# Performance work log

Hardware: AMD Instinct MI355X
Metric: run time of the kernel (lower is better)

Reference implementation:

```python
import jax, jax.numpy as jnp
import numpy as np

PULSE = (0.01, 0.005)
W_RGB, W_INTER, W_DIST, W_HASH = 1.0, 1.0, 0.01, 0.1
NUM_SEGMENTS = 65536
R, N = 4096, 48


def setup_inputs() -> dict:
    key = jax.random.key(0)
    ks = jax.random.split(key, 12)
    M = R * N
    return {
        "pd_rgbs": jax.random.uniform(ks[0], (R, 3), jnp.float32),
        "gt_rgbs": jax.random.uniform(ks[1], (R, 3), jnp.float32),
        "render_sdist": jnp.sort(jax.random.uniform(ks[2], (R, N + 1), jnp.float32), axis=-1),
        "render_weights": jax.random.uniform(ks[3], (R, N), jnp.float32) * 0.05,
        "prop_sdist_0": jnp.sort(jax.random.uniform(ks[4], (R, 257), jnp.float32), axis=-1),
        "prop_weights_0": jax.random.uniform(ks[5], (R, 256), jnp.float32) * 0.02,
        "prop_sdist_1": jnp.sort(jax.random.uniform(ks[6], (R, 97), jnp.float32), axis=-1),
        "prop_weights_1": jax.random.uniform(ks[7], (R, 96), jnp.float32) * 0.02,
        "enc_embds_0": jax.random.normal(ks[8], (M, 2), jnp.float32) * 0.01,
        "enc_embds_1": jax.random.normal(ks[9], (M, 2), jnp.float32) * 0.01,
        "enc_idx_0": jnp.sort(jax.random.randint(ks[10], (M,), 0, NUM_SEGMENTS)),
        "enc_idx_1": jnp.sort(jax.random.randint(ks[11], (M,), 0, NUM_SEGMENTS)),
    }


def blur_step_function(sdist, wnorm, pw):
    # sdist: [R, N+1], wnorm: [R, N]
    cat = jnp.concatenate([sdist - pw, sdist + pw], axis=-1)        # [R, 2N+2]
    sort_idx = jnp.argsort(cat, axis=-1)
    bounds = jnp.take_along_axis(cat, sort_idx, axis=-1)
    z = jnp.zeros_like(wnorm[..., :1])
    diff = jnp.concatenate([wnorm, z], -1) - jnp.concatenate([z, wnorm], -1)  # [R, N+1]
    radio = diff / (2.0 * pw)
    radio_double = jnp.concatenate([radio, -radio], axis=-1)        # [R, 2N+2]
    radio_sorted = jnp.take_along_axis(radio_double, sort_idx[..., :-1], axis=-1)
    ds = bounds[..., 1:] - bounds[..., :-1]                          # [R, 2N+1]
    recover = jnp.maximum(jnp.cumsum(ds * jnp.cumsum(radio_sorted, -1), -1), 0.0)
    blur_w = jnp.concatenate([jnp.zeros_like(recover[..., :1]), recover], -1)  # [R, 2N+2]
    return bounds, blur_w


def sorted_interp_quad(x, xp, fpdf, fcdf):
    # x: [R, X], xp/fpdf/fcdf: [R, P]
    mask = x[..., None, :] >= xp[..., :, None]  # [R, P, X]

    def find_interval(v):
        lo = jnp.where(mask, v[..., None], v[..., :1, None])
        hi = jnp.where(~mask, v[..., None], v[..., -1:, None])
        return lo.max(-2), hi.min(-2), lo.argmax(-2), hi.argmin(-2)

    fcdf0, fcdf1, i0, i1 = find_interval(fcdf)
    fpdf0 = jnp.take_along_axis(fpdf, i0, axis=-1)
    fpdf1 = jnp.take_along_axis(fpdf, i1, axis=-1)
    xp0, xp1, _, _ = find_interval(xp)
    offset = jnp.clip(jnp.nan_to_num((x - xp0) / (xp1 - xp0), nan=0.0), 0.0, 1.0)
    return fcdf0 + (x - xp0) * (fpdf0 + fpdf1 * offset + fpdf0 * (1.0 - offset)) / 2.0


def inter_loss_level(prop_sdist, prop_weights, render_sdist, wnorm, pw):
    dist_b, w_b = blur_step_function(render_sdist, wnorm, pw)
    area = 0.5 * (w_b[..., 1:] + w_b[..., :-1]) * (dist_b[..., 1:] - dist_b[..., :-1])
    cdf = jnp.concatenate([jnp.zeros_like(area[..., :1]), jnp.cumsum(area, -1)], -1)
    cdf_interp = sorted_interp_quad(prop_sdist, dist_b, w_b, cdf)
    w_s = jnp.diff(cdf_interp, axis=-1)
    return jnp.mean(jnp.maximum(w_s - prop_weights, 0.0) ** 2 / (prop_weights + 1e-5))


def distortion_loss(render_weights, render_sdist):
    mid = 0.5 * (render_sdist[..., 1:] + render_sdist[..., :-1])     # [R, N]
    sdist_all = jnp.abs(mid[..., :, None] - mid[..., None, :])       # [R, N, N]
    part1 = jnp.einsum('rn,rnm,rm->r', render_weights, sdist_all, render_weights)
    part2 = jnp.sum(render_weights ** 2 * (render_sdist[..., 1:] - render_sdist[..., :-1]), -1) / 3.0
    return jnp.mean(jnp.abs(part1) + jnp.abs(part2))


def hash_decay_level(param, idx):
    s = jax.ops.segment_sum(param ** 2, idx, num_segments=NUM_SEGMENTS)
    cnt = jax.ops.segment_sum(jnp.ones((param.shape[0], 1), param.dtype), idx, num_segments=NUM_SEGMENTS)
    return jnp.mean(s / jnp.maximum(cnt, 1.0))  # empty segments contribute 0 (like segment_coo mean init=0)


def reference(pd_rgbs, gt_rgbs, render_sdist, render_weights,
              prop_sdist_0, prop_weights_0, prop_sdist_1, prop_weights_1,
              enc_embds_0, enc_embds_1, enc_idx_0, enc_idx_1):
    loss_rgb = jnp.mean((pd_rgbs - gt_rgbs) ** 2)
    wnorm = render_weights / (render_sdist[..., 1:] - render_sdist[..., :-1] + 1e-8)
    loss_inter = (inter_loss_level(prop_sdist_0, prop_weights_0, render_sdist, wnorm, PULSE[0])
                  + inter_loss_level(prop_sdist_1, prop_weights_1, render_sdist, wnorm, PULSE[1]))
    loss_dist = distortion_loss(render_weights, render_sdist)
    loss_hash = hash_decay_level(enc_embds_0, enc_idx_0) + hash_decay_level(enc_embds_1, enc_idx_1)
    return W_RGB * loss_rgb + W_INTER * loss_inter + W_DIST * loss_dist + W_HASH * loss_hash
```

## Files before the change

kernel.cpp:

```cpp
#include <hip/hip_runtime.h>

#define R 4096
#define NN 48
#define NP 49
#define C 98
#define NSEG 65536
#define MM (R * NN)
#define RPB 4
#define GB_ROW (R / RPB)
#define GB_HASH (MM / 256)
#define GRID (GB_ROW + 2 * GB_HASH)

#define WAVE_FENCE() __builtin_amdgcn_wave_barrier()

__device__ __forceinline__ float wscan_add(float v, int lane) {
#pragma unroll
    for (int d = 1; d < 64; d <<= 1) {
        float t = __shfl_up(v, d, 64);
        if (lane >= d) v += t;
    }
    return v;
}

__device__ __forceinline__ int wscan_max(int v, int lane) {
#pragma unroll
    for (int d = 1; d < 64; d <<= 1) {
        int t = __shfl_up(v, d, 64);
        if (lane >= d) v = max(v, t);
    }
    return v;
}

__global__ __launch_bounds__(256) void fused_kernel(
    const float* __restrict__ pd, const float* __restrict__ gt,
    const float* __restrict__ sdist_g, const float* __restrict__ w_g,
    const float* __restrict__ ps0, const float* __restrict__ pwt0,
    const float* __restrict__ ps1, const float* __restrict__ pwt1,
    const float* __restrict__ e0, const int* __restrict__ idx0,
    const float* __restrict__ e1, const int* __restrict__ idx1,
    float* __restrict__ partial)
{
    __shared__ float s_sd[RPB][NP];
    __shared__ float s_wn[RPB][NN];
    __shared__ float s_w[RPB][NN];
    __shared__ float s_mid[RPB][NN];
    __shared__ float s_bounds[RPB][C];
    __shared__ float s_rs[RPB][C];
    __shared__ float s_wb[RPB][C];
    __shared__ float s_cdf[RPB][C];
    __shared__ int   s_fe[RPB][C];
    __shared__ float s_ci[RPB][260];
    __shared__ float s_red[RPB];
    __shared__ unsigned long long s_masks[6];

    const int tid = threadIdx.x;
    const int wid = tid >> 6;
    const int lane = tid & 63;

    if (blockIdx.x >= GB_ROW) {
        const int h = blockIdx.x - GB_ROW;
        const int lvlh = (h >= GB_HASH);
        const float* __restrict__ emb = lvlh ? e1 : e0;
        const int*   __restrict__ idx = lvlh ? idx1 : idx0;
        const int base = (lvlh ? h - GB_HASH : h) * 256;
        const int i = base + tid;

        const int seg = idx[i];
        const int head = (i == 0) || (idx[i - 1] != seg);
        unsigned long long m = __ballot(head);
        if (lane == 0) s_masks[wid + 1] = m;
        if (wid == 0) {
            const int j = base - 64 + lane;
            int hh = 0;
            if (j == 0) hh = 1;
            else if (j > 0) hh = (idx[j - 1] != idx[j]);
            unsigned long long mp = __ballot(hh);
            if (lane == 0) s_masks[0] = mp;
        }
        if (wid == 3) {
            const int j = base + 256 + lane;
            int hh = 1;
            if (j < MM) hh = (idx[j - 1] != idx[j]);
            unsigned long long mn = __ballot(hh);
            if (lane == 0) s_masks[5] = mn;
        }
        __syncthreads();

        const unsigned long long m_prev = s_masks[wid];
        const unsigned long long m_cur  = s_masks[wid + 1];
        const unsigned long long m_next = s_masks[wid + 2];
        const int wb0 = base + (wid << 6);

        const unsigned long long low = m_cur & (~0ULL >> (63 - lane));
        int s;
        if (low) s = wb0 + 63 - __builtin_clzll(low);
        else if (m_prev) s = wb0 - 64 + 63 - __builtin_clzll(m_prev);
        else { s = i; while (s > 0 && idx[s - 1] == seg) --s; }

        const unsigned long long high =
            (lane < 63) ? (m_cur & (~0ULL << (lane + 1))) : 0ULL;
        int e;
        if (high) e = wb0 + __builtin_ctzll(high);
        else if (m_next) e = wb0 + 64 + __builtin_ctzll(m_next);
        else { e = i + 1; while (e < MM && idx[e] == seg) ++e; }

        const float a = emb[2 * i], b = emb[2 * i + 1];
        float v = (a * a + b * b) / (float)(e - s);

#pragma unroll
        for (int d = 32; d > 0; d >>= 1) v += __shfl_down(v, d, 64);
        if (lane == 0) s_red[wid] = v;
        __syncthreads();
        if (tid == 0)
            partial[blockIdx.x] =
                (s_red[0] + s_red[1] + s_red[2] + s_red[3]) *
                (0.1f / ((float)NSEG * 2.f));
        return;
    }

    const int r = blockIdx.x * RPB + wid;

    float* sd  = s_sd[wid];
    float* wn  = s_wn[wid];
    float* w   = s_w[wid];
    float* mid = s_mid[wid];
    float* bounds = s_bounds[wid];
    float* rs  = s_rs[wid];
    float* wb  = s_wb[wid];
    float* cdf = s_cdf[wid];
    int*   fe  = s_fe[wid];
    float* ci  = s_ci[wid];

    if (lane < NP) sd[lane] = sdist_g[r * NP + lane];
    if (lane < NN) w[lane] = w_g[r * NN + lane];
    WAVE_FENCE();
    if (lane < NN) {
        wn[lane]  = w[lane] / (sd[lane + 1] - sd[lane] + 1e-8f);
        mid[lane] = 0.5f * (sd[lane + 1] + sd[lane]);
    }
    WAVE_FENCE();

    float local = 0.f;

#pragma unroll
    for (int lvl = 0; lvl < 2; ++lvl) {
        const float pw = (lvl == 0) ? 0.01f : 0.005f;
        const int X = (lvl == 0) ? 257 : 97;
        const float* ps  = (lvl == 0) ? ps0 : ps1;
        const float* pwt = (lvl == 0) ? pwt0 : pwt1;

        if (lane < NP) {
            const int i = lane;
            const float dlo = (i > 0)  ? wn[i - 1] : 0.f;
            const float dhi = (i < NN) ? wn[i] : 0.f;
            const float rd = (dhi - dlo) / (2.f * pw);
            const float vlo = sd[i] - pw, vhi = sd[i] + pw;
            int lo = 0, hi = NP;
            while (lo < hi) { int m = (lo + hi) >> 1; if (sd[m] + pw < vlo) lo = m + 1; else hi = m; }
            const int rlo = i + lo;
            lo = 0; hi = NP;
            while (lo < hi) { int m = (lo + hi) >> 1; if (sd[m] - pw <= vhi) lo = m + 1; else hi = m; }
            const int rhi = i + lo;
            bounds[rlo] = vlo; rs[rlo] = rd;
            bounds[rhi] = vhi; rs[rhi] = -rd;
        }
        WAVE_FENCE();

        const int k0 = 2 * lane, k1 = 2 * lane + 1;
        const bool v0 = (k0 <= C - 2), v1 = (k1 <= C - 2);
        float b0 = 0.f, b1 = 0.f, b2 = 0.f, r0 = 0.f, r1 = 0.f;
        if (v0) { b0 = bounds[k0]; b1 = bounds[k0 + 1]; r0 = rs[k0]; }
        if (v1) { b2 = bounds[k1 + 1]; r1 = rs[k1]; }
        const float ds0 = b1 - b0, ds1 = b2 - b1;

        float pairv = r0 + r1;
        float incl = wscan_add(pairv, lane);
        float excl = __shfl_up(incl, 1, 64); if (lane == 0) excl = 0.f;
        const float cum0 = excl + r0, cum1 = excl + pairv;

        float y0 = v0 ? ds0 * cum0 : 0.f;
        float y1 = v1 ? ds1 * cum1 : 0.f;
        pairv = y0 + y1;
        incl = wscan_add(pairv, lane);
        excl = __shfl_up(incl, 1, 64); if (lane == 0) excl = 0.f;
        const float rec0 = v0 ? fmaxf(excl + y0, 0.f) : 0.f;
        const float rec1 = v1 ? fmaxf(excl + pairv, 0.f) : 0.f;

        float rprev = __shfl_up(rec1, 1, 64); if (lane == 0) rprev = 0.f;
        float t0 = v0 ? 0.5f * (rec0 + rprev) * ds0 : 0.f;
        float t1 = v1 ? 0.5f * (rec1 + rec0) * ds1 : 0.f;
        pairv = t0 + t1;
        incl = wscan_add(pairv, lane);
        excl = __shfl_up(incl, 1, 64); if (lane == 0) excl = 0.f;
        const float c0 = excl + t0;
        const float c1 = excl + pairv;

        float cprev = __shfl_up(c1, 1, 64); if (lane == 0) cprev = 0.f;
        const int j0 = k0 + 1, j1 = k1 + 1;
        const int m0 = (v0 && c0 != cprev) ? j0 : 0;
        const int m1 = (v1 && c1 != c0) ? j1 : 0;
        int pm = max(m0, m1);
        int inclm = wscan_max(pm, lane);
        int exclm = __shfl_up(inclm, 1, 64); if (lane == 0) exclm = 0;

        if (lane == 0) { wb[0] = 0.f; cdf[0] = 0.f; fe[0] = 0; }
        if (v0) { wb[j0] = rec0; cdf[j0] = c0; fe[j0] = max(exclm, m0); }
        if (v1) { wb[j1] = rec1; cdf[j1] = c1; fe[j1] = max(exclm, pm); }
        const float cdf_last = __shfl(c1, (C - 2) >> 1, 64);
        WAVE_FENCE();

        for (int t = lane; t < X; t += 64) {
            const float x = ps[r * X + t];
            int lo = 0, hi = C;
            while (lo < hi) { int m = (lo + hi) >> 1; if (bounds[m] <= x) lo = m + 1; else hi = m; }
            const int j = lo - 1;
            float res = 0.f;
            if (j >= 0) {
                const float fcdf0 = cdf[j];
                const int   i0   = fe[j];
                const float xp0  = bounds[j];
                float xp1; int i1;
                if (j == C - 1) { xp1 = bounds[C - 1]; i1 = 0; }
                else {
                    xp1 = bounds[j + 1];
                    i1 = (cdf[j + 1] == cdf_last) ? 0 : (j + 1);
                }
                const float fpdf0 = wb[i0], fpdf1 = wb[i1];
                const float dx = x - xp0, den = xp1 - xp0;
                float off;
                if (den != 0.f) off = dx / den;
                else off = (dx == 0.f) ? 0.f : ((dx > 0.f) ? 1.f : 0.f);
                off = fminf(fmaxf(off, 0.f), 1.f);
                res = fcdf0 + dx * (fpdf0 + fpdf1 * off + fpdf0 * (1.f - off)) * 0.5f;
            }
            ci[t] = res;
        }
        WAVE_FENCE();

        float lsum = 0.f;
        for (int t = lane; t < X - 1; t += 64) {
            const float ws = ci[t + 1] - ci[t];
            const float pv = pwt[r * (X - 1) + t];
            const float d = fmaxf(ws - pv, 0.f);
            lsum += d * d / (pv + 1e-5f);
        }
        local += lsum * (1.0f / ((float)R * (float)(X - 1)));
        WAVE_FENCE();
    }

    float p1 = 0.f;
    for (int t = lane; t < NN * NN; t += 64) {
        const int n = t / NN, m2 = t - n * NN;
        p1 += w[n] * w[m2] * fabsf(mid[n] - mid[m2]);
    }
    local += p1 * (0.01f / (float)R);
    if (lane < NN) {
        const float dd = sd[lane + 1] - sd[lane];
        local += (w[lane] * w[lane] * dd) * (0.01f / (3.f * (float)R));
    }

    if (lane < 3) {
        const float e = pd[r * 3 + lane] - gt[r * 3 + lane];
        local += e * e * (1.0f / ((float)R * 3.f));
    }

#pragma unroll
    for (int d = 32; d > 0; d >>= 1) local += __shfl_down(local, d, 64);
    if (lane == 0) s_red[wid] = local;
    __syncthreads();
    if (tid == 0)
        partial[blockIdx.x] = s_red[0] + s_red[1] + s_red[2] + s_red[3];
}

__global__ __launch_bounds__(256) void reduce_kernel(
    const float* __restrict__ partial, float* __restrict__ out)
{
    float s = 0.f;
    for (int t = threadIdx.x; t < GRID; t += 256) s += partial[t];
    const int lane = threadIdx.x & 63;
#pragma unroll
    for (int d = 32; d > 0; d >>= 1) s += __shfl_down(s, d, 64);
    __shared__ float sred[4];
    if (lane == 0) sred[threadIdx.x >> 6] = s;
    __syncthreads();
    if (threadIdx.x == 0)
        out[0] = sred[0] + sred[1] + sred[2] + sred[3];
}

extern "C" void kernel_launch(void* const* d_in, const int* in_sizes, int n_in,
                              void* d_out, int out_size, void* d_ws, size_t ws_size,
                              hipStream_t stream)
{
    const float* pd  = (const float*)d_in[0];
    const float* gt  = (const float*)d_in[1];
    const float* sd  = (const float*)d_in[2];
    const float* w   = (const float*)d_in[3];
    const float* ps0 = (const float*)d_in[4];
    const float* pw0 = (const float*)d_in[5];
    const float* ps1 = (const float*)d_in[6];
    const float* pw1 = (const float*)d_in[7];
    const float* e0  = (const float*)d_in[8];
    const float* e1  = (const float*)d_in[9];
    const int* i0    = (const int*)d_in[10];
    const int* i1    = (const int*)d_in[11];

    float* partial = (float*)d_ws;

    hipLaunchKernelGGL(fused_kernel, dim3(GRID), dim3(256), 0, stream,
                       pd, gt, sd, w, ps0, pw0, ps1, pw1,
                       e0, i0, e1, i1, partial);
    hipLaunchKernelGGL(reduce_kernel, dim3(1), dim3(256), 0, stream,
                       partial, (float*)d_out);
}
```

Before: 107.3 us.

## Use prefix-sum distortion loss, branchless binary searches, and batched interpolation lookups

```diff
diff --git a/kernel.cpp b/kernel.cpp
--- a/kernel.cpp
+++ b/kernel.cpp
@@ -42,8 +42,6 @@
 {
     __shared__ float s_sd[RPB][NP];
     __shared__ float s_wn[RPB][NN];
-    __shared__ float s_w[RPB][NN];
-    __shared__ float s_mid[RPB][NN];
     __shared__ float s_bounds[RPB][C];
     __shared__ float s_rs[RPB][C];
     __shared__ float s_wb[RPB][C];
@@ -122,8 +120,6 @@
 
     float* sd  = s_sd[wid];
     float* wn  = s_wn[wid];
-    float* w   = s_w[wid];
-    float* mid = s_mid[wid];
     float* bounds = s_bounds[wid];
     float* rs  = s_rs[wid];
     float* wb  = s_wb[wid];
@@ -132,11 +128,12 @@
     float* ci  = s_ci[wid];
 
     if (lane < NP) sd[lane] = sdist_g[r * NP + lane];
-    if (lane < NN) w[lane] = w_g[r * NN + lane];
+    const float w_l = (lane < NN) ? w_g[r * NN + lane] : 0.f;
     WAVE_FENCE();
+    float mid_l = 0.f;
     if (lane < NN) {
-        wn[lane]  = w[lane] / (sd[lane + 1] - sd[lane] + 1e-8f);
-        mid[lane] = 0.5f * (sd[lane + 1] + sd[lane]);
+        wn[lane] = w_l / (sd[lane + 1] - sd[lane] + 1e-8f);
+        mid_l    = 0.5f * (sd[lane + 1] + sd[lane]);
     }
     WAVE_FENCE();
 
@@ -146,6 +143,7 @@
     for (int lvl = 0; lvl < 2; ++lvl) {
         const float pw = (lvl == 0) ? 0.01f : 0.005f;
         const int X = (lvl == 0) ? 257 : 97;
+        const int NPASS = (lvl == 0) ? 5 : 2;
         const float* ps  = (lvl == 0) ? ps0 : ps1;
         const float* pwt = (lvl == 0) ? pwt0 : pwt1;
 
@@ -155,14 +153,17 @@
             const float dhi = (i < NN) ? wn[i] : 0.f;
             const float rd = (dhi - dlo) / (2.f * pw);
             const float vlo = sd[i] - pw, vhi = sd[i] + pw;
-            int lo = 0, hi = NP;
-            while (lo < hi) { int m = (lo + hi) >> 1; if (sd[m] + pw < vlo) lo = m + 1; else hi = m; }
-            const int rlo = i + lo;
-            lo = 0; hi = NP;
-            while (lo < hi) { int m = (lo + hi) >> 1; if (sd[m] - pw <= vhi) lo = m + 1; else hi = m; }
-            const int rhi = i + lo;
-            bounds[rlo] = vlo; rs[rlo] = rd;
-            bounds[rhi] = vhi; rs[rhi] = -rd;
+            unsigned p1 = 0, p2 = 0;
+#pragma unroll
+            for (unsigned step = 32; step; step >>= 1) {
+                unsigned n1 = p1 + step, n2 = p2 + step;
+                float a1 = sd[(n1 <= NP ? n1 : NP) - 1];
+                float a2 = sd[(n2 <= NP ? n2 : NP) - 1];
+                if (n1 <= NP && a1 + pw < vlo)  p1 = n1;
+                if (n2 <= NP && a2 - pw <= vhi) p2 = n2;
+            }
+            bounds[i + p1] = vlo; rs[i + p1] = rd;
+            bounds[i + p2] = vhi; rs[i + p2] = -rd;
         }
         WAVE_FENCE();
 
@@ -209,54 +210,95 @@
         const float cdf_last = __shfl(c1, (C - 2) >> 1, 64);
         WAVE_FENCE();
 
-        for (int t = lane; t < X; t += 64) {
-            const float x = ps[r * X + t];
-            int lo = 0, hi = C;
-            while (lo < hi) { int m = (lo + hi) >> 1; if (bounds[m] <= x) lo = m + 1; else hi = m; }
-            const int j = lo - 1;
-            float res = 0.f;
-            if (j >= 0) {
-                const float fcdf0 = cdf[j];
-                const int   i0   = fe[j];
-                const float xp0  = bounds[j];
-                float xp1; int i1;
-                if (j == C - 1) { xp1 = bounds[C - 1]; i1 = 0; }
-                else {
-                    xp1 = bounds[j + 1];
-                    i1 = (cdf[j + 1] == cdf_last) ? 0 : (j + 1);
+        {
+            float xv[5];
+            int   jv[5];
+#pragma unroll
+            for (int p = 0; p < NPASS; ++p) {
+                const int t = p * 64 + lane;
+                const int tc = t < X ? t : X - 1;
+                xv[p] = ps[r * X + tc];
+            }
+#pragma unroll
+            for (unsigned step = 64; step; step >>= 1) {
+#pragma unroll
+                for (int p = 0; p < NPASS; ++p) {
+                    unsigned pos = (unsigned)(p == 0 ? 0 : 0);
                 }
-                const float fpdf0 = wb[i0], fpdf1 = wb[i1];
-                const float dx = x - xp0, den = xp1 - xp0;
-                float off;
-                if (den != 0.f) off = dx / den;
-                else off = (dx == 0.f) ? 0.f : ((dx > 0.f) ? 1.f : 0.f);
-                off = fminf(fmaxf(off, 0.f), 1.f);
-                res = fcdf0 + dx * (fpdf0 + fpdf1 * off + fpdf0 * (1.f - off)) * 0.5f;
-            }
-            ci[t] = res;
+            }
+            unsigned posv[5];
+#pragma unroll
+            for (int p = 0; p < NPASS; ++p) posv[p] = 0u;
+#pragma unroll
+            for (unsigned step = 64; step; step >>= 1) {
+#pragma unroll
+                for (int p = 0; p < NPASS; ++p) {
+                    const unsigned np_ = posv[p] + step;
+                    const float bv = bounds[(np_ <= C ? np_ : C) - 1];
+                    if (np_ <= C && bv <= xv[p]) posv[p] = np_;
+                }
+            }
+#pragma unroll
+            for (int p = 0; p < NPASS; ++p) jv[p] = (int)posv[p] - 1;
+
+#pragma unroll
+            for (int p = 0; p < NPASS; ++p) {
+                const int t = p * 64 + lane;
+                const float x = xv[p];
+                const int j = jv[p];
+                float res = 0.f;
+                if (j >= 0) {
+                    const float fcdf0 = cdf[j];
+                    const int   i0   = fe[j];
+                    const float xp0  = bounds[j];
+                    float xp1; int i1;
+                    if (j == C - 1) { xp1 = bounds[C - 1]; i1 = 0; }
+                    else {
+                        xp1 = bounds[j + 1];
+                        i1 = (cdf[j + 1] == cdf_last) ? 0 : (j + 1);
+                    }
+                    const float fpdf0 = wb[i0], fpdf1 = wb[i1];
+                    const float dx = x - xp0, den = xp1 - xp0;
+                    float off;
+                    if (den != 0.f) off = dx / den;
+                    else off = (dx == 0.f) ? 0.f : ((dx > 0.f) ? 1.f : 0.f);
+                    off = fminf(fmaxf(off, 0.f), 1.f);
+                    res = fcdf0 + dx * (fpdf0 + fpdf1 * off + fpdf0 * (1.f - off)) * 0.5f;
+                }
+                if (t < X) ci[t] = res;
+            }
         }
         WAVE_FENCE();
 
         float lsum = 0.f;
-        for (int t = lane; t < X - 1; t += 64) {
-            const float ws = ci[t + 1] - ci[t];
-            const float pv = pwt[r * (X - 1) + t];
-            const float d = fmaxf(ws - pv, 0.f);
-            lsum += d * d / (pv + 1e-5f);
+#pragma unroll
+        for (int p = 0; p < NPASS; ++p) {
+            const int t = p * 64 + lane;
+            if (t < X - 1) {
+                const float ws = ci[t + 1] - ci[t];
+                const float pv = pwt[r * (X - 1) + t];
+                const float d = fmaxf(ws - pv, 0.f);
+                lsum += d * d / (pv + 1e-5f);
+            }
         }
         local += lsum * (1.0f / ((float)R * (float)(X - 1)));
         WAVE_FENCE();
     }
 
-    float p1 = 0.f;
-    for (int t = lane; t < NN * NN; t += 64) {
-        const int n = t / NN, m2 = t - n * NN;
-        p1 += w[n] * w[m2] * fabsf(mid[n] - mid[m2]);
-    }
-    local += p1 * (0.01f / (float)R);
-    if (lane < NN) {
-        const float dd = sd[lane + 1] - sd[lane];
-        local += (w[lane] * w[lane] * dd) * (0.01f / (3.f * (float)R));
+    {
+        const float wm = w_l * mid_l;
+        const float P = wscan_add(w_l, lane);
+        const float Q = wscan_add(wm, lane);
+        const float W = __shfl(P, 63, 64);
+        const float TQ = __shfl(Q, 63, 64);
+        float term = 0.f;
+        if (lane < NN)
+            term = w_l * (mid_l * (2.f * P - W) - 2.f * Q + TQ);
+        local += term * (0.01f / (float)R);
+        if (lane < NN) {
+            const float dd = sd[lane + 1] - sd[lane];
+            local += (w_l * w_l * dd) * (0.01f / (3.f * (float)R));
+        }
     }
 
     if (lane < 3) {
```

Result: faster. 103.1 us (-3.9%).
